# Kernel optimization log

Measured on AMD Instinct MI355X. Metric: run time of the kernel, lower is better.

## Reference

```python
import jax, jax.numpy as jnp
import numpy as np

B, S, D = 1, 4096, 2048
H, KVH, HD = 16, 4, 128  # heads, kv heads, head_dim
ROPE_BASE = 10000.0


def _rope_cos_sin(position_ids):
    # inv_freq: [HD/2]
    inv_freq = 1.0 / (ROPE_BASE ** (jnp.arange(0, HD, 2, dtype=jnp.float32) / HD))
    # freqs: [B, S, HD/2] -> emb: [B, S, HD] (concat(freqs, freqs))
    freqs = position_ids.astype(jnp.float32)[..., None] * inv_freq
    emb = jnp.concatenate([freqs, freqs], axis=-1)
    # [B, 1, S, HD] to broadcast over heads
    return jnp.cos(emb)[:, None, :, :], jnp.sin(emb)[:, None, :, :]


def _rotate_half(x):
    x1, x2 = x[..., : HD // 2], x[..., HD // 2 :]
    return jnp.concatenate([-x2, x1], axis=-1)


def setup_inputs() -> dict:
    key = jax.random.key(0)
    ks = jax.random.split(key, 5)
    s = 0.02
    return {
        "hidden_states": jax.random.normal(ks[0], (B, S, D), jnp.float32),
        "Wq": jax.random.normal(ks[1], (H * HD, D), jnp.float32) * s,
        "Wk": jax.random.normal(ks[2], (KVH * HD, D), jnp.float32) * s,
        "Wv": jax.random.normal(ks[3], (KVH * HD, D), jnp.float32) * s,
        "Wo": jax.random.normal(ks[4], (D, H * HD), jnp.float32) * s,
        "position_ids": jnp.arange(S, dtype=jnp.int64 if jax.config.jax_enable_x64 else jnp.int32)[None, :].repeat(B, 0),
    }


def reference(hidden_states, Wq, Wk, Wv, Wo, position_ids):
    b, s, _ = hidden_states.shape
    # projections (no bias): [b, s, nheads*hd] -> [b, nh, s, hd]
    q = (hidden_states @ Wq.T).reshape(b, s, H, HD).transpose(0, 2, 1, 3)
    k = (hidden_states @ Wk.T).reshape(b, s, KVH, HD).transpose(0, 2, 1, 3)
    v = (hidden_states @ Wv.T).reshape(b, s, KVH, HD).transpose(0, 2, 1, 3)

    cos, sin = _rope_cos_sin(position_ids)  # [b,1,s,hd]
    q = q * cos + _rotate_half(q) * sin
    k = k * cos + _rotate_half(k) * sin

    # GQA: repeat kv heads (repeat_interleave along head dim)
    n_rep = H // KVH
    k = jnp.repeat(k, n_rep, axis=1)
    v = jnp.repeat(v, n_rep, axis=1)

    # eager quadratic attention with causal mask
    scores = jnp.einsum("bhqd,bhkd->bhqk", q, k) / jnp.sqrt(jnp.float32(HD))
    causal = jnp.tril(jnp.ones((s, s), dtype=bool))
    scores = jnp.where(causal[None, None], scores, jnp.finfo(scores.dtype).min)
    attn = jax.nn.softmax(scores, axis=-1)
    out = jnp.einsum("bhqk,bhkd->bhqd", attn, v)  # [b,h,s,hd]
    out = out.transpose(0, 2, 1, 3).reshape(b, s, H * HD)
    return out @ Wo.T
```

## Files before the change

kernel.cpp:

```cpp
#include <hip/hip_runtime.h>
#include <hip/hip_bf16.h>

constexpr int S   = 4096;
constexpr int D   = 2048;
constexpr int H   = 16;
constexpr int KVH = 4;
constexpr int HD  = 128;

using short8 = __attribute__((ext_vector_type(8))) short;
using f32x4  = __attribute__((ext_vector_type(4))) float;
using f32x16 = __attribute__((ext_vector_type(16))) float;

__device__ inline ushort f2bf(float f) {
  union { float f; unsigned u; } x{f};
  unsigned r = x.u + 0x7FFFu + ((x.u >> 16) & 1u);
  return (ushort)(r >> 16);
}
__device__ inline float bf2f(ushort h) {
  union { unsigned u; float f; } x{(unsigned)h << 16};
  return x.f;
}
__device__ inline unsigned pkbf(float a, float b) {
  union { float f; unsigned u; } xa{a}, xb{b};
  unsigned ra = xa.u + 0x7FFFu + ((xa.u >> 16) & 1u);
  unsigned rb = xb.u + 0x7FFFu + ((xb.u >> 16) & 1u);
#if __has_builtin(__builtin_amdgcn_perm)
  return __builtin_amdgcn_perm(rb, ra, 0x07060302u);
#else
  return (rb & 0xFFFF0000u) | (ra >> 16);
#endif
}
__device__ inline unsigned pkbf_t(float a, float b) {
  union { float f; unsigned u; } xa{a}, xb{b};
#if __has_builtin(__builtin_amdgcn_perm)
  return __builtin_amdgcn_perm(xb.u, xa.u, 0x07060302u);
#else
  return (xb.u & 0xFFFF0000u) | (xa.u >> 16);
#endif
}
__device__ inline float fast_exp2(float x) {
#if __has_builtin(__builtin_amdgcn_exp2f)
  return __builtin_amdgcn_exp2f(x);
#else
  return exp2f(x);
#endif
}

__device__ inline void async_copy16(const ushort* g, ushort* l) {
  __builtin_amdgcn_global_load_lds(
      (const __attribute__((address_space(1))) unsigned int*)g,
      (__attribute__((address_space(3))) unsigned int*)l, 16, 0, 0);
}

constexpr size_t N_HID = (size_t)S * D;
constexpr size_t N_WQ  = (size_t)(H * HD) * D;
constexpr size_t N_WKV = (size_t)(KVH * HD) * D;
constexpr size_t C1_ = N_HID;
constexpr size_t C2_ = C1_ + N_WQ;
constexpr size_t C3_ = C2_ + N_WKV;
constexpr size_t C4_ = C3_ + N_WKV;
constexpr size_t C5_ = C4_ + N_WQ;

__global__ void cvt_all_kernel(const float* __restrict__ hid, const float* __restrict__ wq,
                               const float* __restrict__ wk, const float* __restrict__ wv,
                               const float* __restrict__ wo, ushort* __restrict__ dst) {
  size_t i = (size_t)blockIdx.x * blockDim.x + threadIdx.x;
  size_t off = i * 4;
  if (off >= C5_) return;
  const float* src;
  if      (off < C1_) src = hid + off;
  else if (off < C2_) src = wq + (off - C1_);
  else if (off < C3_) src = wk + (off - C2_);
  else if (off < C4_) src = wv + (off - C3_);
  else                src = wo + (off - C4_);
  float4 f = *(const float4*)src;
  ushort4 o;
  o.x = f2bf(f.x); o.y = f2bf(f.y); o.z = f2bf(f.z); o.w = f2bf(f.w);
  *(ushort4*)&dst[off] = o;
}

template <int OUT_MODE>
__device__ __forceinline__ void gemm_tile(const ushort* __restrict__ A,
                                          const ushort* __restrict__ Bt,
                                          void* __restrict__ Cv,
                                          int M, int N, int K, int bxi, int byi,
                                          ushort* As, ushort* Bs) {
  const int bm = byi * 128;
  const int bn = bxi * 128;
  const int tid  = threadIdx.x;
  const int lane = tid & 63;
  const int w    = tid >> 6;
  const int wr = w >> 1, wc = w & 1;
  const int lm = lane & 15, quad = lane >> 4;

  f32x4 acc[4][4];
#pragma unroll
  for (int i = 0; i < 4; ++i)
#pragma unroll
    for (int j = 0; j < 4; ++j) acc[i][j] = (f32x4){0.f, 0.f, 0.f, 0.f};

  for (int k0 = 0; k0 < K; k0 += 32) {
#pragma unroll
    for (int j = 0; j < 2; ++j) {
      int idx = j * 256 + tid;
      int row = idx >> 2;
      int col = (idx & 3) * 8;
      int ubase = (j * 256 + w * 64) * 8;
      async_copy16(A + (size_t)(bm + row) * K + k0 + col, &As[ubase]);
      async_copy16(Bt + (size_t)(bn + row) * K + k0 + col, &Bs[ubase]);
    }
    __syncthreads();
    short8 af[4], bfr[4];
#pragma unroll
    for (int t = 0; t < 4; ++t) {
      af[t]  = *(const short8*)&As[(wr * 64 + t * 16 + lm) * 32 + quad * 8];
      bfr[t] = *(const short8*)&Bs[(wc * 64 + t * 16 + lm) * 32 + quad * 8];
    }
#pragma unroll
    for (int i = 0; i < 4; ++i)
#pragma unroll
      for (int j = 0; j < 4; ++j)
        acc[i][j] = __builtin_amdgcn_mfma_f32_16x16x32_bf16(af[i], bfr[j], acc[i][j], 0, 0, 0);
    __syncthreads();
  }

#pragma unroll
  for (int i = 0; i < 4; ++i)
#pragma unroll
    for (int j = 0; j < 4; ++j) {
      if (OUT_MODE == 2) {
        int col  = bn + wc * 64 + j * 16 + lm;
        int rowb = bm + wr * 64 + i * 16 + quad * 4;
        ushort4 o4;
        o4.x = f2bf(acc[i][j][0]); o4.y = f2bf(acc[i][j][1]);
        o4.z = f2bf(acc[i][j][2]); o4.w = f2bf(acc[i][j][3]);
        *(ushort4*)&((ushort*)Cv)[(size_t)col * M + rowb] = o4;
      } else {
#pragma unroll
        for (int r = 0; r < 4; ++r) {
          size_t row = bm + wr * 64 + i * 16 + quad * 4 + r;
          size_t col = bn + wc * 64 + j * 16 + lm;
          if (OUT_MODE == 1) ((ushort*)Cv)[row * N + col] = f2bf(acc[i][j][r]);
          else               ((float*)Cv)[row * N + col]  = acc[i][j][r];
        }
      }
    }
}

__global__ __launch_bounds__(256) void gemm_qkv_kernel(const ushort* __restrict__ hb,
                                                       const ushort* __restrict__ wq,
                                                       const ushort* __restrict__ wk,
                                                       const ushort* __restrict__ wv,
                                                       ushort* __restrict__ qb,
                                                       ushort* __restrict__ kb,
                                                       ushort* __restrict__ vtb) {
  __shared__ __align__(16) ushort As[128 * 32];
  __shared__ __align__(16) ushort Bs[128 * 32];
  int bid = blockIdx.x;
  if (bid < 512) {
    gemm_tile<1>(hb, wq, qb, S, H * HD, D, bid & 15, bid >> 4, As, Bs);
  } else if (bid < 640) {
    int b = bid - 512;
    gemm_tile<1>(hb, wk, kb, S, KVH * HD, D, b & 3, b >> 2, As, Bs);
  } else {
    int b = bid - 640;
    gemm_tile<2>(hb, wv, vtb, S, KVH * HD, D, b & 3, b >> 2, As, Bs);
  }
}

template <int OUT_MODE>
__global__ __launch_bounds__(256) void gemm_bt_kernel(const ushort* __restrict__ A,
                                                      const ushort* __restrict__ Bt,
                                                      void* __restrict__ Cv,
                                                      int M, int N, int K) {
  __shared__ __align__(16) ushort As[128 * 32];
  __shared__ __align__(16) ushort Bs[128 * 32];
  gemm_tile<OUT_MODE>(A, Bt, Cv, M, N, K, blockIdx.x, blockIdx.y, As, Bs);
}

__global__ void rope_bf16_kernel(ushort* __restrict__ qb, ushort* __restrict__ kb,
                                 const int* __restrict__ pos_ids) {
  int idx = blockIdx.x * blockDim.x + threadIdx.x;
  const int total = S * (H + KVH) * (HD / 2);
  if (idx >= total) return;
  int j = idx & 63;
  int t = idx >> 6;
  int head = t % (H + KVH);
  int s = t / (H + KVH);
  float p = (float)pos_ids[s];
  float inv_freq = exp2f(-(float)j * (13.287712379549449f / 64.0f));
  float ang = p * inv_freq;
  float c = cosf(ang), sn = sinf(ang);
  ushort* base = (head < H) ? (qb + (size_t)s * (H * HD) + head * HD)
                            : (kb + (size_t)s * (KVH * HD) + (head - H) * HD);
  float x1 = bf2f(base[j]), x2 = bf2f(base[j + 64]);
  base[j]      = f2bf(x1 * c - x2 * sn);
  base[j + 64] = f2bf(x2 * c + x1 * sn);
}

__global__ __launch_bounds__(512) void attn_mfma_kernel(const ushort* __restrict__ q,
                                                        const ushort* __restrict__ k,
                                                        const ushort* __restrict__ Vt,
                                                        ushort* __restrict__ o) {
  const int bid = blockIdx.x;
  const int h   = bid & 15;
  const int t   = bid >> 4;
  const int qi  = 31 - t;
  const int q0  = qi * 128;
  const int kvh = h >> 2;
  const int tid  = threadIdx.x;
  const int lane = tid & 63;
  const int w    = tid >> 6;
  const int qw   = w >> 1;
  const int ks   = w & 1;
  const int m32  = lane & 31;
  const int p    = lane >> 5;

  __shared__ __align__(16) ushort LDSu[32768];

  const int q0w = q0 + qw * 32;

  short8 qf[8];
#pragma unroll
  for (int s = 0; s < 8; ++s)
    qf[s] = *(const short8*)&q[(size_t)(q0w + m32) * (H * HD) + h * HD + s * 16 + p * 8];

  f32x16 Oacc[4];
#pragma unroll
  for (int i = 0; i < 4; ++i)
#pragma unroll
    for (int r = 0; r < 16; ++r) Oacc[i][r] = 0.f;
  float ls4[4] = {0.f, 0.f, 0.f, 0.f};

  auto stage = [&](int k0s, int buf) {
#pragma unroll
    for (int i = 0; i < 4; ++i) {
      int c = w * 4 + i;
      if (c < 16) {
        int kh = c >> 3, s = c & 7;
        async_copy16(&k[(size_t)(k0s + kh * 32 + m32) * (KVH * HD) + kvh * HD + s * 16 + p * 8],
                     &LDSu[buf * 8192 + c * 512]);
      } else {
        int cv = c - 16;
        int ht = cv >> 2, t2 = cv & 3;
        async_copy16(&Vt[(size_t)(kvh * HD + ht * 32 + m32) * S + k0s + t2 * 16 + p * 8],
                     &LDSu[16384 + buf * 8192 + cv * 512]);
      }
    }
  };

  stage(0, 0);
  __syncthreads();

  const float C1  = 0.08838834764831845f * 1.4426950408889634f;
  const float F2n = -12.0f * 1.4426950408889634f;
  const int T = 2 * qi + 2;

  for (int tt = 0; tt < T; ++tt) {
    const int k0  = tt * 64;
    const int cur = tt & 1;
    if (tt + 1 < T) stage(k0 + 64, cur ^ 1);
    const ushort* Kb = &LDSu[cur * 8192];
    const ushort* Vb = &LDSu[16384 + cur * 8192];

    const int kbase = k0 + ks * 32;
    if (kbase <= q0w + 31) {
      f32x16 stA, stB;
#pragma unroll
      for (int r = 0; r < 16; ++r) { stA[r] = 0.f; stB[r] = 0.f; }
#pragma unroll
      for (int s = 0; s < 8; s += 2) {
        short8 kf0 = *(const short8*)&Kb[(ks * 8 + s) * 512 + lane * 8];
        short8 kf1 = *(const short8*)&Kb[(ks * 8 + s + 1) * 512 + lane * 8];
        stA = __builtin_amdgcn_mfma_f32_32x32x16_bf16(kf0, qf[s], stA, 0, 0, 0);
        stB = __builtin_amdgcn_mfma_f32_32x32x16_bf16(kf1, qf[s + 1], stB, 0, 0, 0);
      }

      float pv[16];
      if (kbase == q0w) {
#pragma unroll
        for (int r = 0; r < 16; ++r) {
          int kvl = (r & 3) + 8 * (r >> 2) + 4 * p;
          float e = fast_exp2(fmaf(stA[r] + stB[r], C1, F2n));
          e = (kvl > m32) ? 0.f : e;
          pv[r] = e; ls4[r & 3] += e;
        }
      } else {
#pragma unroll
        for (int r = 0; r < 16; ++r) {
          float e = fast_exp2(fmaf(stA[r] + stB[r], C1, F2n));
          pv[r] = e; ls4[r & 3] += e;
        }
      }

      unsigned own2[4][2], oth[4][2];
#pragma unroll
      for (int g = 0; g < 4; ++g) {
        own2[g][0] = pkbf_t(pv[4 * g + 0], pv[4 * g + 1]);
        own2[g][1] = pkbf_t(pv[4 * g + 2], pv[4 * g + 3]);
        oth[g][0]  = __shfl_xor(own2[g][0], 32);
        oth[g][1]  = __shfl_xor(own2[g][1], 32);
      }
      short8 pf[2];
#pragma unroll
      for (int t2 = 0; t2 < 2; ++t2) {
        union { unsigned u4[4]; short8 s8; } pb;
        pb.u4[0] = p ? oth[2 * t2 + 1][0] : own2[2 * t2][0];
        pb.u4[1] = p ? oth[2 * t2 + 1][1] : own2[2 * t2][1];
        pb.u4[2] = p ? own2[2 * t2 + 1][0] : oth[2 * t2][0];
        pb.u4[3] = p ? own2[2 * t2 + 1][1] : oth[2 * t2][1];
        pf[t2] = pb.s8;
      }

#pragma unroll
      for (int ht = 0; ht < 4; ++ht)
#pragma unroll
        for (int t2l = 0; t2l < 2; ++t2l) {
          int cv = ht * 4 + ks * 2 + t2l;
          short8 vf = *(const short8*)&Vb[cv * 512 + lane * 8];
          Oacc[ht] = __builtin_amdgcn_mfma_f32_32x32x16_bf16(vf, pf[t2l], Oacc[ht], 0, 0, 0);
        }
    }
    __syncthreads();
  }

  float lsum = (ls4[0] + ls4[1]) + (ls4[2] + ls4[3]);
  float* mb = (float*)LDSu;

  if (ks) mb[(qw << 6) | lane] = lsum;
  __syncthreads();
  if (!ks) lsum += mb[(qw << 6) | lane];
  __syncthreads();

  if (ks) {
    float* base = mb + qw * 4096;
#pragma unroll
    for (int ht = 0; ht < 4; ++ht)
#pragma unroll
      for (int r = 0; r < 16; ++r)
        base[ht * 1024 + r * 64 + lane] = Oacc[ht][r];
  }
  __syncthreads();

  if (!ks) {
    const float* base = mb + qw * 4096;
#pragma unroll
    for (int ht = 0; ht < 4; ++ht)
#pragma unroll
      for (int r = 0; r < 16; ++r)
        Oacc[ht][r] += base[ht * 1024 + r * 64 + lane];

    float ltot = lsum + __shfl_xor(lsum, 32);
    float inv = 1.0f / ltot;
#pragma unroll
    for (int ht = 0; ht < 4; ++ht)
#pragma unroll
      for (int rq = 0; rq < 4; ++rq) {
        uint2 dd;
        dd.x = pkbf(Oacc[ht][4 * rq + 0] * inv, Oacc[ht][4 * rq + 1] * inv);
        dd.y = pkbf(Oacc[ht][4 * rq + 2] * inv, Oacc[ht][4 * rq + 3] * inv);
        *(uint2*)&o[(size_t)(q0w + m32) * (H * HD) + h * HD + ht * 32 + 8 * rq + 4 * p] = dd;
      }
  }
}

extern "C" void kernel_launch(void* const* d_in, const int* in_sizes, int n_in,
                              void* d_out, int out_size, void* d_ws, size_t ws_size,
                              hipStream_t stream) {
  const float* hidden = (const float*)d_in[0];
  const float* Wq     = (const float*)d_in[1];
  const float* Wk     = (const float*)d_in[2];
  const float* Wv     = (const float*)d_in[3];
  const float* Wo     = (const float*)d_in[4];
  const int*   pos    = (const int*)d_in[5];
  float* out = (float*)d_out;

  ushort* hb  = (ushort*)d_ws;
  ushort* wqb = hb  + N_HID;
  ushort* wkb = wqb + N_WQ;
  ushort* wvb = wkb + N_WKV;
  ushort* wob = wvb + N_WKV;
  ushort* qb  = wob + N_WQ;
  ushort* kb  = qb  + (size_t)S * (H * HD);
  ushort* vtb = kb  + (size_t)S * (KVH * HD);
  ushort* ob  = vtb + (size_t)(KVH * HD) * S;

  dim3 blk(256);
  size_t n4 = C5_ / 4;
  cvt_all_kernel<<<(int)((n4 + 255) / 256), blk, 0, stream>>>(hidden, Wq, Wk, Wv, Wo, hb);

  gemm_qkv_kernel<<<dim3(768), blk, 0, stream>>>(hb, wqb, wkb, wvb, qb, kb, vtb);

  int rope_total = S * (H + KVH) * (HD / 2);
  rope_bf16_kernel<<<(rope_total + 255) / 256, blk, 0, stream>>>(qb, kb, pos);

  attn_mfma_kernel<<<dim3(512), dim3(512), 0, stream>>>(qb, kb, vtb, ob);

  gemm_bt_kernel<0><<<dim3(D / 128, S / 128), blk, 0, stream>>>(ob, wob, out, S, D, D);
}
```

Measured before the change: 348.1 us.

## Interleave causal tile order, precompute staging pointers, raise priority around MFMA

Block-to-query-tile mapping changes from strictly longest-first to an alternating scheme that pairs long and short causal tiles, so work per CU is better balanced. The K/V staging lambda now uses a per-wave base pointer computed once and advanced by a fixed stride, removing per-iteration index arithmetic and branching. s_setprio brackets the QK and PV MFMA loops so waves issuing matrix ops get scheduling priority over waves doing softmax work. The new tile ordering gives up the pure longest-first schedule, which could hurt tail behaviour depending on how blocks are dispatched.

```diff
diff --git a/kernel.cpp b/kernel.cpp
--- a/kernel.cpp
+++ b/kernel.cpp
@@ -205,7 +205,8 @@
   const int bid = blockIdx.x;
   const int h   = bid & 15;
   const int t   = bid >> 4;
-  const int qi  = 31 - t;
+  const int tl  = t & 15, hi2 = t >> 4;
+  const int qi  = hi2 ? (2 * tl) : (31 - 2 * tl);
   const int q0  = qi * 128;
   const int kvh = h >> 2;
   const int tid  = threadIdx.x;
@@ -232,24 +233,29 @@
     for (int r = 0; r < 16; ++r) Oacc[i][r] = 0.f;
   float ls4[4] = {0.f, 0.f, 0.f, 0.f};
 
-  auto stage = [&](int k0s, int buf) {
-#pragma unroll
-    for (int i = 0; i < 4; ++i) {
-      int c = w * 4 + i;
-      if (c < 16) {
-        int kh = c >> 3, s = c & 7;
-        async_copy16(&k[(size_t)(k0s + kh * 32 + m32) * (KVH * HD) + kvh * HD + s * 16 + p * 8],
-                     &LDSu[buf * 8192 + c * 512]);
-      } else {
-        int cv = c - 16;
-        int ht = cv >> 2, t2 = cv & 3;
-        async_copy16(&Vt[(size_t)(kvh * HD + ht * 32 + m32) * S + k0s + t2 * 16 + p * 8],
-                     &LDSu[16384 + buf * 8192 + cv * 512]);
-      }
-    }
+  const ushort* gsrc0;
+  unsigned ldoff;
+  size_t gstep;
+  if (w < 4) {
+    const int c0 = w * 4, kh = c0 >> 3, s0 = c0 & 7;
+    gsrc0 = &k[(size_t)(kh * 32 + m32) * (KVH * HD) + kvh * HD + s0 * 16 + p * 8];
+    ldoff = c0 * 512;
+    gstep = (size_t)64 * (KVH * HD);
+  } else {
+    const int cv0 = (w - 4) * 4, ht = cv0 >> 2;
+    gsrc0 = &Vt[(size_t)(kvh * HD + ht * 32 + m32) * S + p * 8];
+    ldoff = 16384u + cv0 * 512;
+    gstep = 64;
+  }
+  auto stage = [&](int buf) {
+    const unsigned lb = ldoff + (buf ? 8192u : 0u);
+#pragma unroll
+    for (int i = 0; i < 4; ++i)
+      async_copy16(gsrc0 + i * 16, &LDSu[lb + i * 512]);
+    gsrc0 += gstep;
   };
 
-  stage(0, 0);
+  stage(0);
   __syncthreads();
 
   const float C1  = 0.08838834764831845f * 1.4426950408889634f;
@@ -259,7 +265,7 @@
   for (int tt = 0; tt < T; ++tt) {
     const int k0  = tt * 64;
     const int cur = tt & 1;
-    if (tt + 1 < T) stage(k0 + 64, cur ^ 1);
+    if (tt + 1 < T) stage(cur ^ 1);
     const ushort* Kb = &LDSu[cur * 8192];
     const ushort* Vb = &LDSu[16384 + cur * 8192];
 
@@ -268,6 +274,7 @@
       f32x16 stA, stB;
 #pragma unroll
       for (int r = 0; r < 16; ++r) { stA[r] = 0.f; stB[r] = 0.f; }
+      __builtin_amdgcn_s_setprio(1);
 #pragma unroll
       for (int s = 0; s < 8; s += 2) {
         short8 kf0 = *(const short8*)&Kb[(ks * 8 + s) * 512 + lane * 8];
@@ -275,6 +282,7 @@
         stA = __builtin_amdgcn_mfma_f32_32x32x16_bf16(kf0, qf[s], stA, 0, 0, 0);
         stB = __builtin_amdgcn_mfma_f32_32x32x16_bf16(kf1, qf[s + 1], stB, 0, 0, 0);
       }
+      __builtin_amdgcn_s_setprio(0);
 
       float pv[16];
       if (kbase == q0w) {
@@ -312,6 +320,7 @@
         pf[t2] = pb.s8;
       }
 
+      __builtin_amdgcn_s_setprio(1);
 #pragma unroll
       for (int ht = 0; ht < 4; ++ht)
 #pragma unroll
@@ -320,6 +329,7 @@
           short8 vf = *(const short8*)&Vb[cv * 512 + lane * 8];
           Oacc[ht] = __builtin_amdgcn_mfma_f32_32x32x16_bf16(vf, pf[t2l], Oacc[ht], 0, 0, 0);
         }
+      __builtin_amdgcn_s_setprio(0);
     }
     __syncthreads();
   }
```

Result: slower. 380.7 us (+9.4%).
